# Kernel tuning notes

Measured on AMD Instinct MI355X. Metric: run time of the kernel, lower is better.

The kernel has to match this reference:

```python
import jax, jax.numpy as jnp
import numpy as np

N_NODES = 100000
N_EDGES = 1600000
D_IN = 128
CH = [128, 128]
N_GRAPHS = 256


def _glorot(key, shape):
    lim = float(np.sqrt(6.0 / (shape[0] + shape[1])))
    return jax.random.uniform(key, shape, jnp.float32, -lim, lim)


def setup_inputs() -> dict:
    key = jax.random.key(0)
    ks = jax.random.split(key, 12)
    x = jax.random.normal(ks[0], (N_NODES, D_IN), jnp.float32)
    edge_index = jax.random.randint(ks[1], (2, N_EDGES), 0, N_NODES, jnp.int64)
    batch = jnp.sort(jax.random.randint(ks[2], (N_NODES,), 0, N_GRAPHS, jnp.int64))
    W1 = _glorot(ks[3], (D_IN, CH[0]))
    b1 = jnp.zeros((CH[0],), jnp.float32)
    W2 = _glorot(ks[4], (CH[0], CH[1]))
    b2 = jnp.zeros((CH[1],), jnp.float32)
    Wm1 = _glorot(ks[5], (CH[1], 500)); bm1 = jnp.zeros((500,), jnp.float32)
    Wm2 = _glorot(ks[6], (500, 100));   bm2 = jnp.zeros((100,), jnp.float32)
    Wm3 = _glorot(ks[7], (100, 1));     bm3 = jnp.zeros((1,), jnp.float32)
    return {"x": x, "edge_index": edge_index, "batch": batch,
            "W1": W1, "b1": b1, "W2": W2, "b2": b2,
            "Wm1": Wm1, "bm1": bm1, "Wm2": Wm2, "bm2": bm2,
            "Wm3": Wm3, "bm3": bm3}


def gcn_conv(x, W, b, src, dst, n_nodes):
    # GCNConv with add_self_loops=True, symmetric normalization.
    h = x @ W  # [N, C]
    deg = jnp.zeros((n_nodes,), h.dtype).at[dst].add(1.0) + 1.0  # +1 self loop
    dinv = jax.lax.rsqrt(deg)  # deg >= 1
    norm = dinv[src] * dinv[dst]  # [E]
    agg = jnp.zeros_like(h).at[dst].add(h[src] * norm[:, None])
    agg = agg + h * (dinv * dinv)[:, None]  # self-loop term, norm = dinv[i]^2
    return agg + b


def global_mean_pool(x, batch, n_graphs):
    s = jax.ops.segment_sum(x, batch, num_segments=n_graphs)
    cnt = jax.ops.segment_sum(jnp.ones((x.shape[0],), x.dtype), batch, num_segments=n_graphs)
    return s / jnp.maximum(cnt, 1.0)[:, None]


def reference(x, edge_index, batch, W1, b1, W2, b2, Wm1, bm1, Wm2, bm2, Wm3, bm3):
    src, dst = edge_index[0], edge_index[1]
    h = jax.nn.relu(gcn_conv(x, W1, b1, src, dst, N_NODES))
    h = jax.nn.relu(gcn_conv(h, W2, b2, src, dst, N_NODES))
    g = global_mean_pool(h, batch, N_GRAPHS)  # [G, CH1]
    g = jax.nn.relu(g @ Wm1 + bm1)
    g = jax.nn.relu(g @ Wm2 + bm2)
    return g @ Wm3 + bm3  # [G, 1]
```

## Files before the change

### kernel.cpp

```cpp
#include <hip/hip_runtime.h>

#define CDIM 128
#define NGRAPH 256
#define BSH 7
#define BCAP 4096
#define NBLK 256

typedef unsigned short bf16_t;
typedef __attribute__((ext_vector_type(8))) short bf16x8;
typedef __attribute__((ext_vector_type(4))) float f32x4;

__device__ __forceinline__ float bflo(unsigned u) { return __uint_as_float(u << 16); }
__device__ __forceinline__ float bfhi(unsigned u) { return __uint_as_float(u & 0xffff0000u); }
__device__ __forceinline__ unsigned short f2bf(float f) {
  unsigned u = __float_as_uint(f);
  u += 0x7fffu + ((u >> 16) & 1u);
  return (unsigned short)(u >> 16);
}

__global__ __launch_bounds__(1024) void k_phist(const int* __restrict__ dst,
    int* __restrict__ phist, const float* __restrict__ W1,
    const float* __restrict__ W2, bf16_t* __restrict__ Wtg1,
    bf16_t* __restrict__ Wtg2, float* __restrict__ gb, int E, int NB) {
  __shared__ int hist[1024];
  int t = blockIdx.x, tid = threadIdx.x;
  int gidx = t * 1024 + tid;
  if (gidx < 16384) {
    int n = gidx >> 7, k = gidx & 127;
    Wtg1[n * 128 + k] = f2bf(W1[k * 128 + n]);
    Wtg2[n * 128 + k] = f2bf(W2[k * 128 + n]);
  }
  if (gidx < NGRAPH * CDIM) gb[gidx] = 0.f;
  for (int i = tid; i < NB; i += 1024) hist[i] = 0;
  __syncthreads();
  int tile = (E + NBLK - 1) / NBLK;
  int lo = t * tile;
  int hi = lo + tile; if (hi > E) hi = E;
  for (int i = lo + tid; i < hi; i += 1024) atomicAdd(&hist[dst[i] >> BSH], 1);
  __syncthreads();
  for (int i = tid; i < NB; i += 1024) phist[i * NBLK + t] = hist[i];
}

__global__ __launch_bounds__(256) void k_bscan(int* __restrict__ phist,
    int* __restrict__ btot) {
  __shared__ int wsum[4];
  int b = blockIdx.x;
  int tid = threadIdx.x, lane = tid & 63, wave = tid >> 6;
  int orig = phist[b * NBLK + tid];
  int v = orig;
#pragma unroll
  for (int ofs = 1; ofs < 64; ofs <<= 1) {
    int u = __shfl_up(v, ofs, 64);
    if (lane >= ofs) v += u;
  }
  if (lane == 63) wsum[wave] = v;
  __syncthreads();
  int add = 0;
#pragma unroll
  for (int w = 0; w < 3; w++) if (w < wave) add += wsum[w];
  int incl = v + add;
  phist[b * NBLK + tid] = incl - orig;
  if (tid == 255) btot[b] = incl;
}

__global__ __launch_bounds__(1024) void k_boff(const int* __restrict__ bsums,
    int* __restrict__ boffs, int G) {
  __shared__ int sh[1024];
  int tid = threadIdx.x;
  int v = (tid < G) ? bsums[tid] : 0;
  sh[tid] = v;
  __syncthreads();
  for (int ofs = 1; ofs < 1024; ofs <<= 1) {
    int u = (tid >= ofs) ? sh[tid - ofs] : 0;
    __syncthreads();
    sh[tid] += u;
    __syncthreads();
  }
  if (tid < G) boffs[tid] = sh[tid] - v;
  if (tid == G) boffs[G] = (G > 0) ? sh[G - 1] : 0;
}

__global__ __launch_bounds__(1024) void k_pscatter(const int* __restrict__ src,
    const int* __restrict__ dst, const int* __restrict__ phist,
    const int* __restrict__ bbase, unsigned* __restrict__ tmp, int E, int NB) {
  __shared__ int cur[1024];
  int t = blockIdx.x, tid = threadIdx.x;
  for (int i = tid; i < NB; i += 1024) cur[i] = bbase[i] + phist[i * NBLK + t];
  __syncthreads();
  int tile = (E + NBLK - 1) / NBLK;
  int lo = t * tile;
  int hi = lo + tile; if (hi > E) hi = E;
  for (int i = lo + tid; i < hi; i += 1024) {
    int d = dst[i];
    int p = atomicAdd(&cur[d >> BSH], 1);
    tmp[p] = (unsigned)src[i] | ((unsigned)(d & 127) << 20);
  }
}

__global__ __launch_bounds__(256) void k_csort2(const unsigned* __restrict__ tmp,
    const int* __restrict__ bbase, int* __restrict__ rowptr, float* __restrict__ dinv,
    int* __restrict__ col, int N, int NB, int E) {
  __shared__ int hist[128];
  __shared__ int sc[128];
  __shared__ int lcur[128];
  __shared__ unsigned buf[BCAP];
  int b = blockIdx.x;
  int n0 = b << BSH;
  int base = bbase[b];
  int cnt = bbase[b + 1] - base;
  int tid = threadIdx.x;
  if (tid < 128) hist[tid] = 0;
  __syncthreads();
  for (int i = tid; i < cnt; i += 256) atomicAdd(&hist[(tmp[base + i] >> 20) & 127], 1);
  __syncthreads();
  if (tid < 128) sc[tid] = hist[tid];
  __syncthreads();
  for (int ofs = 1; ofs < 128; ofs <<= 1) {
    int v = (tid < 128 && tid >= ofs) ? sc[tid - ofs] : 0;
    __syncthreads();
    if (tid < 128) sc[tid] += v;
    __syncthreads();
  }
  if (tid < 128) {
    int excl = sc[tid] - hist[tid];
    lcur[tid] = excl;
    int node = n0 + tid;
    if (node < N) {
      rowptr[node] = base + excl;
      dinv[node] = rsqrtf((float)hist[tid] + 1.0f);
    }
  }
  if (b == 0 && tid == 0) rowptr[N] = E;
  __syncthreads();
  if (cnt <= BCAP) {
    for (int i = tid; i < cnt; i += 256) {
      unsigned pk = tmp[base + i];
      int p = atomicAdd(&lcur[(pk >> 20) & 127], 1);
      buf[p] = pk & 0xFFFFFu;
    }
    __syncthreads();
    for (int i = tid; i < cnt; i += 256) col[base + i] = (int)buf[i];
  } else {
    for (int i = tid; i < cnt; i += 256) {
      unsigned pk = tmp[base + i];
      int p = atomicAdd(&lcur[(pk >> 20) & 127], 1);
      col[base + p] = (int)(pk & 0xFFFFFu);
    }
  }
}

#define WSTRIDE 136
template <int BF16IN>
__global__ __launch_bounds__(256) void k_gemm(const void* __restrict__ Ap,
    const bf16_t* __restrict__ Wtg, bf16_t* __restrict__ Co, int M) {
  __shared__ bf16_t Wt[128 * WSTRIDE];
  int tid = threadIdx.x;
  for (int c2 = tid; c2 < 2048; c2 += 256) {
    int n = c2 >> 4;
    int k8 = (c2 & 15) << 3;
    *(uint4*)&Wt[n * WSTRIDE + k8] = *(const uint4*)&Wtg[n * 128 + k8];
  }
  __syncthreads();

  int wave = tid >> 6;
  int lane = tid & 63;
  int m = lane & 15;
  int q = lane >> 4;
  int nstrips = (M + 63) >> 6;

  for (int s = blockIdx.x; s < nstrips; s += gridDim.x) {
    int rowA = s * 64 + wave * 16 + m;
    if (rowA > M - 1) rowA = M - 1;
    bf16x8 a[4];
#pragma unroll
    for (int c = 0; c < 4; c++) {
      if (BF16IN) {
        a[c] = *(const bf16x8*)((const bf16_t*)Ap + (size_t)rowA * CDIM + c * 32 + q * 8);
      } else {
        const float* ap = (const float*)Ap + (size_t)rowA * CDIM + c * 32 + q * 8;
        float4 f0 = *(const float4*)ap;
        float4 f1 = *(const float4*)(ap + 4);
        union { bf16x8 v; unsigned short u[8]; } ua;
        ua.u[0] = f2bf(f0.x); ua.u[1] = f2bf(f0.y); ua.u[2] = f2bf(f0.z); ua.u[3] = f2bf(f0.w);
        ua.u[4] = f2bf(f1.x); ua.u[5] = f2bf(f1.y); ua.u[6] = f2bf(f1.z); ua.u[7] = f2bf(f1.w);
        a[c] = ua.v;
      }
    }
#pragma unroll
    for (int t = 0; t < 8; t++) {
      f32x4 acc = {0.f, 0.f, 0.f, 0.f};
#pragma unroll
      for (int c = 0; c < 4; c++) {
        bf16x8 bv = *(const bf16x8*)&Wt[(t * 16 + m) * WSTRIDE + c * 32 + q * 8];
        acc = __builtin_amdgcn_mfma_f32_16x16x32_bf16(a[c], bv, acc, 0, 0, 0);
      }
#pragma unroll
      for (int r = 0; r < 4; r++) {
        int row = s * 64 + wave * 16 + q * 4 + r;
        if (row < M) Co[(size_t)row * CDIM + t * 16 + m] = f2bf(acc[r]);
      }
    }
  }
}

__global__ __launch_bounds__(256) void k_agg0(const bf16_t* __restrict__ t,
    const int* __restrict__ rowptr, const int* __restrict__ col,
    const float* __restrict__ dinv, const float* __restrict__ bias,
    bf16_t* __restrict__ out, int N) {
  int wave = threadIdx.x >> 6;
  int lane = threadIdx.x & 63;
  int node = blockIdx.x * 4 + wave;
  if (node >= N) return;
  const unsigned* tp = (const unsigned*)t;
  float di = dinv[node];
  unsigned sv = tp[(size_t)node * 64 + lane];
  float a0 = bflo(sv) * di;
  float a1 = bfhi(sv) * di;
  int beg = rowptr[node], end = rowptr[node + 1];
  for (int base = beg; base < end; base += 64) {
    int cnt = end - base; if (cnt > 64) cnt = 64;
    int sL = 0, wLi = 0;
    if (lane < cnt) { int s = col[base + lane]; sL = s; wLi = __float_as_int(dinv[s]); }
    int cnt8 = (cnt + 7) & ~7;
    for (int j = 0; j < cnt8; j += 8) {
      int ss[8]; float ww[8]; unsigned vv[8];
#pragma unroll
      for (int u = 0; u < 8; u++) {
        ss[u] = __builtin_amdgcn_readlane(sL, j + u);
        ww[u] = __int_as_float(__builtin_amdgcn_readlane(wLi, j + u));
      }
#pragma unroll
      for (int u = 0; u < 8; u++) vv[u] = tp[(size_t)ss[u] * 64 + lane];
#pragma unroll
      for (int u = 0; u < 8; u++) {
        a0 = fmaf(bflo(vv[u]), ww[u], a0);
        a1 = fmaf(bfhi(vv[u]), ww[u], a1);
      }
    }
  }
  float2 bb = ((const float2*)bias)[lane];
  float o0 = fmaxf(fmaf(di, a0, bb.x), 0.f);
  float o1 = fmaxf(fmaf(di, a1, bb.y), 0.f);
  ((unsigned*)out)[(size_t)node * 64 + lane] =
      ((unsigned)f2bf(o1) << 16) | f2bf(o0);
}

__global__ __launch_bounds__(256) void k_aggp(const bf16_t* __restrict__ t,
    const int* __restrict__ rowptr, const int* __restrict__ col,
    const float* __restrict__ dinv, const float* __restrict__ bias,
    const int* __restrict__ batch, float* __restrict__ gsum, int N) {
  int wave = threadIdx.x >> 6;
  int lane = threadIdx.x & 63;
  int n0 = (blockIdx.x * 4 + wave) * 16;
  if (n0 >= N) return;
  int nEnd = n0 + 16; if (nEnd > N) nEnd = N;
  const unsigned* tp = (const unsigned*)t;
  float2 bb = ((const float2*)bias)[lane];
  float p0 = 0.f, p1 = 0.f;
  int curb = batch[n0];

  for (int node = n0; node < nEnd; node++) {
    float di = dinv[node];
    unsigned sv = tp[(size_t)node * 64 + lane];
    float a0 = bflo(sv) * di;
    float a1 = bfhi(sv) * di;
    int beg = rowptr[node], end = rowptr[node + 1];
    for (int base = beg; base < end; base += 64) {
      int cnt = end - base; if (cnt > 64) cnt = 64;
      int sL = 0, wLi = 0;
      if (lane < cnt) { int s = col[base + lane]; sL = s; wLi = __float_as_int(dinv[s]); }
      int cnt8 = (cnt + 7) & ~7;
      for (int j = 0; j < cnt8; j += 8) {
        int ss[8]; float ww[8]; unsigned vv[8];
#pragma unroll
        for (int u = 0; u < 8; u++) {
          ss[u] = __builtin_amdgcn_readlane(sL, j + u);
          ww[u] = __int_as_float(__builtin_amdgcn_readlane(wLi, j + u));
        }
#pragma unroll
        for (int u = 0; u < 8; u++) vv[u] = tp[(size_t)ss[u] * 64 + lane];
#pragma unroll
        for (int u = 0; u < 8; u++) {
          a0 = fmaf(bflo(vv[u]), ww[u], a0);
          a1 = fmaf(bfhi(vv[u]), ww[u], a1);
        }
      }
    }
    float o0 = fmaxf(fmaf(di, a0, bb.x), 0.f);
    float o1 = fmaxf(fmaf(di, a1, bb.y), 0.f);
    int b = batch[node];
    if (b != curb) {
      atomicAdd(&gsum[curb * CDIM + 2 * lane], p0);
      atomicAdd(&gsum[curb * CDIM + 2 * lane + 1], p1);
      curb = b; p0 = p1 = 0.f;
    }
    p0 += __uint_as_float((unsigned)f2bf(o0) << 16);
    p1 += __uint_as_float((unsigned)f2bf(o1) << 16);
  }
  atomicAdd(&gsum[curb * CDIM + 2 * lane], p0);
  atomicAdd(&gsum[curb * CDIM + 2 * lane + 1], p1);
}

__global__ __launch_bounds__(512) void k_mlp(const float* __restrict__ g,
    const int* __restrict__ batch, int N,
    const float* __restrict__ Wm1, const float* __restrict__ bm1,
    const float* __restrict__ Wm2, const float* __restrict__ bm2,
    const float* __restrict__ wm3, const float* __restrict__ bm3,
    float* __restrict__ out) {
  __shared__ float gs[CDIM];
  __shared__ float m1s[500];
  __shared__ float m2s[100];
  int bi = blockIdx.x, tid = threadIdx.x;
  if (tid < CDIM) {
    int lo = 0, hi = N;
    while (lo < hi) { int mid = (lo + hi) >> 1; if (batch[mid] < bi) lo = mid + 1; else hi = mid; }
    int s = lo;
    lo = 0; hi = N;
    int key = bi + 1;
    while (lo < hi) { int mid = (lo + hi) >> 1; if (batch[mid] < key) lo = mid + 1; else hi = mid; }
    float inv = 1.f / fmaxf((float)(lo - s), 1.f);
    gs[tid] = g[bi * CDIM + tid] * inv;
  }
  __syncthreads();
  if (tid < 500) {
    float acc = bm1[tid];
#pragma unroll 4
    for (int k = 0; k < CDIM; k++) acc = fmaf(gs[k], Wm1[k * 500 + tid], acc);
    m1s[tid] = fmaxf(acc, 0.f);
  }
  __syncthreads();
  if (tid < 100) {
    float acc = bm2[tid];
    for (int k = 0; k < 500; k++) acc = fmaf(m1s[k], Wm2[k * 100 + tid], acc);
    m2s[tid] = fmaxf(acc, 0.f) * wm3[tid];
  }
  __syncthreads();
  if (tid < 64) {
    float v = m2s[tid] + ((tid + 64 < 100) ? m2s[tid + 64] : 0.f);
#pragma unroll
    for (int ofs = 32; ofs > 0; ofs >>= 1) v += __shfl_down(v, ofs, 64);
    if (tid == 0) out[bi] = v + bm3[0];
  }
}

static inline size_t align_up(size_t v) { return (v + 255) & ~(size_t)255; }

extern "C" void kernel_launch(void* const* d_in, const int* in_sizes, int n_in,
                              void* d_out, int out_size, void* d_ws, size_t ws_size,
                              hipStream_t stream) {
  const float* x   = (const float*)d_in[0];
  const int*   ei  = (const int*)d_in[1];
  const int*   bat = (const int*)d_in[2];
  const float* W1  = (const float*)d_in[3];
  const float* b1  = (const float*)d_in[4];
  const float* W2  = (const float*)d_in[5];
  const float* b2  = (const float*)d_in[6];
  const float* Wm1 = (const float*)d_in[7];
  const float* bm1 = (const float*)d_in[8];
  const float* Wm2 = (const float*)d_in[9];
  const float* bm2 = (const float*)d_in[10];
  const float* Wm3 = (const float*)d_in[11];
  const float* bm3 = (const float*)d_in[12];
  float* out = (float*)d_out;

  const int E = in_sizes[1] / 2;
  const int N = in_sizes[2];
  const int* src = ei;
  const int* dst = ei + E;
  const int NB = (N + 127) >> BSH;
  const int M  = NB * NBLK;

  char* p = (char*)d_ws;
  bf16_t* t    = (bf16_t*)p;   p += align_up((size_t)N * CDIM * 2);
  bf16_t* h    = (bf16_t*)p;   p += align_up((size_t)N * CDIM * 2);
  int* rowptr  = (int*)p;      p += align_up((size_t)(N + 1) * 4);
  int* colx    = (int*)p;      p += align_up((size_t)E * 4);
  unsigned* tmp= (unsigned*)p; p += align_up((size_t)E * 4);
  float* dinv  = (float*)p;    p += align_up((size_t)N * 4);
  int* phist   = (int*)p;      p += align_up((size_t)M * 4);
  int* btot    = (int*)p;      p += align_up((size_t)NB * 4);
  int* bbase   = (int*)p;      p += align_up((size_t)(NB + 1) * 4);
  bf16_t* Wtg1 = (bf16_t*)p;   p += align_up((size_t)CDIM * CDIM * 2);
  bf16_t* Wtg2 = (bf16_t*)p;   p += align_up((size_t)CDIM * CDIM * 2);
  float* gb    = (float*)p;    p += align_up((size_t)NGRAPH * CDIM * 4);
  (void)ws_size; (void)n_in; (void)out_size;

  k_phist<<<NBLK, 1024, 0, stream>>>(dst, phist, W1, W2, Wtg1, Wtg2, gb, E, NB);
  k_bscan<<<NB, 256, 0, stream>>>(phist, btot);
  k_boff<<<1, 1024, 0, stream>>>(btot, bbase, NB);
  k_pscatter<<<NBLK, 1024, 0, stream>>>(src, dst, phist, bbase, tmp, E, NB);
  k_csort2<<<NB, 256, 0, stream>>>(tmp, bbase, rowptr, dinv, colx, N, NB, E);

  k_gemm<0><<<512, 256, 0, stream>>>(x, Wtg1, t, N);
  k_agg0<<<(N + 3) / 4, 256, 0, stream>>>(t, rowptr, colx, dinv, b1, h, N);
  k_gemm<1><<<512, 256, 0, stream>>>(h, Wtg2, t, N);
  int pwaves = (N + 15) / 16;
  k_aggp<<<(pwaves + 3) / 4, 256, 0, stream>>>(t, rowptr, colx, dinv, b2,
                                               bat, gb, N);
  k_mlp<<<NGRAPH, 512, 0, stream>>>(gb, bat, N, Wm1, bm1, Wm2, bm2, Wm3, bm3, out);
}
```

Baseline: 336.0 us.

## Software-pipeline gather loads in aggregation kernels and prefetch next node's edges

Both aggregation kernels now double-buffer their 8-neighbor gather batches, so loads for the next batch are issued before the FMAs on the current batch, keeping more memory requests in flight. k_aggp also prefetches the next node's rowptr, dinv, self-feature and column/weight lanes while the current node is processed. It halves the nodes handled per wave (16 to 8), which doubles the wave count. The extra live registers for two buffers may lower occupancy, and the smaller per-wave node count means more atomic flushes to the pooled sums.

```diff
diff --git a/kernel.cpp b/kernel.cpp
--- a/kernel.cpp
+++ b/kernel.cpp
@@ -202,6 +202,26 @@
     }
   }
 }
+
+#define GISS(S, W, V, JJ) \
+  { _Pragma("unroll") for (int u = 0; u < 8; u++) { \
+      S[u] = __builtin_amdgcn_readlane(sL, (JJ) + u); \
+      W[u] = __int_as_float(__builtin_amdgcn_readlane(wLi, (JJ) + u)); } \
+    _Pragma("unroll") for (int u = 0; u < 8; u++) \
+      V[u] = tp[(size_t)S[u] * 64 + lane]; }
+#define GCON(W, V) \
+  { _Pragma("unroll") for (int u = 0; u < 8; u++) { \
+      a0 = fmaf(bflo(V[u]), W[u], a0); a1 = fmaf(bfhi(V[u]), W[u], a1); } }
+#define GBLOCK(CNT) \
+  { int nb = ((CNT) + 7) >> 3; \
+    GISS(sA, wA, vA, 0); \
+    int b_ = 1; \
+    for (; b_ + 1 < nb; b_ += 2) { \
+      GISS(sB, wB, vB, b_ * 8);       GCON(wA, vA); \
+      GISS(sA, wA, vA, (b_ + 1) * 8); GCON(wB, vB); \
+    } \
+    if (b_ < nb) { GISS(sB, wB, vB, b_ * 8); GCON(wA, vA); GCON(wB, vB); } \
+    else { GCON(wA, vA); } }
 
 __global__ __launch_bounds__(256) void k_agg0(const bf16_t* __restrict__ t,
     const int* __restrict__ rowptr, const int* __restrict__ col,
@@ -217,26 +237,13 @@
   float a0 = bflo(sv) * di;
   float a1 = bfhi(sv) * di;
   int beg = rowptr[node], end = rowptr[node + 1];
+  int sA[8]; float wA[8]; unsigned vA[8];
+  int sB[8]; float wB[8]; unsigned vB[8];
   for (int base = beg; base < end; base += 64) {
     int cnt = end - base; if (cnt > 64) cnt = 64;
     int sL = 0, wLi = 0;
     if (lane < cnt) { int s = col[base + lane]; sL = s; wLi = __float_as_int(dinv[s]); }
-    int cnt8 = (cnt + 7) & ~7;
-    for (int j = 0; j < cnt8; j += 8) {
-      int ss[8]; float ww[8]; unsigned vv[8];
-#pragma unroll
-      for (int u = 0; u < 8; u++) {
-        ss[u] = __builtin_amdgcn_readlane(sL, j + u);
-        ww[u] = __int_as_float(__builtin_amdgcn_readlane(wLi, j + u));
-      }
-#pragma unroll
-      for (int u = 0; u < 8; u++) vv[u] = tp[(size_t)ss[u] * 64 + lane];
-#pragma unroll
-      for (int u = 0; u < 8; u++) {
-        a0 = fmaf(bflo(vv[u]), ww[u], a0);
-        a1 = fmaf(bfhi(vv[u]), ww[u], a1);
-      }
-    }
+    GBLOCK(cnt);
   }
   float2 bb = ((const float2*)bias)[lane];
   float o0 = fmaxf(fmaf(di, a0, bb.x), 0.f);
@@ -251,40 +258,45 @@
     const int* __restrict__ batch, float* __restrict__ gsum, int N) {
   int wave = threadIdx.x >> 6;
   int lane = threadIdx.x & 63;
-  int n0 = (blockIdx.x * 4 + wave) * 16;
+  int n0 = (blockIdx.x * 4 + wave) * 8;
   if (n0 >= N) return;
-  int nEnd = n0 + 16; if (nEnd > N) nEnd = N;
+  int nEnd = n0 + 8; if (nEnd > N) nEnd = N;
   const unsigned* tp = (const unsigned*)t;
   float2 bb = ((const float2*)bias)[lane];
   float p0 = 0.f, p1 = 0.f;
   int curb = batch[n0];
+  int sA[8]; float wA[8]; unsigned vA[8];
+  int sB[8]; float wB[8]; unsigned vB[8];
+
+  int beg = rowptr[n0], end = rowptr[n0 + 1];
+  float di = dinv[n0];
+  unsigned sv = tp[(size_t)n0 * 64 + lane];
+  int sL = 0, wLi = 0;
+  { int c0 = end - beg; if (c0 > 64) c0 = 64;
+    if (lane < c0) { int s = col[beg + lane]; sL = s; wLi = __float_as_int(dinv[s]); } }
 
   for (int node = n0; node < nEnd; node++) {
-    float di = dinv[node];
-    unsigned sv = tp[(size_t)node * 64 + lane];
     float a0 = bflo(sv) * di;
     float a1 = bfhi(sv) * di;
-    int beg = rowptr[node], end = rowptr[node + 1];
-    for (int base = beg; base < end; base += 64) {
+    int nn = node + 1;
+    int begN = 0, endN = 0, sLN = 0, wLiN = 0;
+    float diN = 0.f; unsigned svN = 0;
+    if (nn < nEnd) {
+      begN = rowptr[nn]; endN = rowptr[nn + 1];
+      diN = dinv[nn];
+      svN = tp[(size_t)nn * 64 + lane];
+      int c0 = endN - begN; if (c0 > 64) c0 = 64;
+      if (lane < c0) { int s = col[begN + lane]; sLN = s; wLiN = __float_as_int(dinv[s]); }
+    }
+    {
+      int cnt = end - beg; if (cnt > 64) cnt = 64;
+      GBLOCK(cnt);
+    }
+    for (int base = beg + 64; base < end; base += 64) {
       int cnt = end - base; if (cnt > 64) cnt = 64;
-      int sL = 0, wLi = 0;
+      sL = 0; wLi = 0;
       if (lane < cnt) { int s = col[base + lane]; sL = s; wLi = __float_as_int(dinv[s]); }
-      int cnt8 = (cnt + 7) & ~7;
-      for (int j = 0; j < cnt8; j += 8) {
-        int ss[8]; float ww[8]; unsigned vv[8];
-#pragma unroll
-        for (int u = 0; u < 8; u++) {
-          ss[u] = __builtin_amdgcn_readlane(sL, j + u);
-          ww[u] = __int_as_float(__builtin_amdgcn_readlane(wLi, j + u));
-        }
-#pragma unroll
-        for (int u = 0; u < 8; u++) vv[u] = tp[(size_t)ss[u] * 64 + lane];
-#pragma unroll
-        for (int u = 0; u < 8; u++) {
-          a0 = fmaf(bflo(vv[u]), ww[u], a0);
-          a1 = fmaf(bfhi(vv[u]), ww[u], a1);
-        }
-      }
+      GBLOCK(cnt);
     }
     float o0 = fmaxf(fmaf(di, a0, bb.x), 0.f);
     float o1 = fmaxf(fmaf(di, a1, bb.y), 0.f);
@@ -296,6 +308,7 @@
     }
     p0 += __uint_as_float((unsigned)f2bf(o0) << 16);
     p1 += __uint_as_float((unsigned)f2bf(o1) << 16);
+    beg = begN; end = endN; di = diN; sv = svN; sL = sLN; wLi = wLiN;
   }
   atomicAdd(&gsum[curb * CDIM + 2 * lane], p0);
   atomicAdd(&gsum[curb * CDIM + 2 * lane + 1], p1);
@@ -394,7 +407,7 @@
   k_gemm<0><<<512, 256, 0, stream>>>(x, Wtg1, t, N);
   k_agg0<<<(N + 3) / 4, 256, 0, stream>>>(t, rowptr, colx, dinv, b1, h, N);
   k_gemm<1><<<512, 256, 0, stream>>>(h, Wtg2, t, N);
-  int pwaves = (N + 15) / 16;
+  int pwaves = (N + 7) / 8;
   k_aggp<<<(pwaves + 3) / 4, 256, 0, stream>>>(t, rowptr, colx, dinv, b2,
                                                bat, gb, N);
   k_mlp<<<NGRAPH, 512, 0, stream>>>(gb, bat, N, Wm1, bm1, Wm2, bm2, Wm3, bm3, out);
```

Result: no change. 341.6 us (+1.7%).

## Split aggregation into feature slices with half-wave edge pairing and persistent grid

Applied to the files above, without the earlier changes.

Both aggregation kernels now run each wave on a 64-column feature slice, chosen by block parity, so each 128-byte row read is half as wide. Each half-wave handles alternate edges and the two halves are combined with a cross-lane shuffle. Gathers are software-pipelined with double-buffered register sets, and the launch becomes a fixed 2048-block grid-stride loop. The aim is more memory-level parallelism and better cache locality per feature slice. The cost is that every node's neighbor indices and dinv values are read twice, once per slice, plus extra shuffle and readlane work.

```diff
diff --git a/kernel.cpp b/kernel.cpp
--- a/kernel.cpp
+++ b/kernel.cpp
@@ -203,46 +203,69 @@
   }
 }
 
+#define GISS(W, V, JJ) \
+  { _Pragma("unroll") for (int r = 0; r < 4; r++) { \
+      int e0 = (JJ) + 2 * r; \
+      int sa = __builtin_amdgcn_readlane(sL, e0); \
+      int sb = __builtin_amdgcn_readlane(sL, e0 + 1); \
+      int wa = __builtin_amdgcn_readlane(wLi, e0); \
+      int wb = __builtin_amdgcn_readlane(wLi, e0 + 1); \
+      int se = g ? sb : sa; \
+      W[r] = __int_as_float(g ? wb : wa); \
+      V[r] = tp2[(size_t)se * 64 + widx]; \
+  } }
+#define GCON(W, V) \
+  { _Pragma("unroll") for (int r = 0; r < 4; r++) { \
+      a0 = fmaf(bflo(V[r]), W[r], a0); a1 = fmaf(bfhi(V[r]), W[r], a1); } }
+#define GBLOCK(CNT) \
+  { int nb_ = ((CNT) + 7) >> 3; \
+    GISS(wA, vA, 0); \
+    int b_ = 1; \
+    for (; b_ + 1 < nb_; b_ += 2) { \
+      GISS(wB, vB, b_ * 8);       GCON(wA, vA); \
+      GISS(wA, vA, (b_ + 1) * 8); GCON(wB, vB); \
+    } \
+    if (b_ < nb_) { GISS(wB, vB, b_ * 8); GCON(wA, vA); GCON(wB, vB); } \
+    else { GCON(wA, vA); } }
+
 __global__ __launch_bounds__(256) void k_agg0(const bf16_t* __restrict__ t,
     const int* __restrict__ rowptr, const int* __restrict__ col,
     const float* __restrict__ dinv, const float* __restrict__ bias,
     bf16_t* __restrict__ out, int N) {
   int wave = threadIdx.x >> 6;
   int lane = threadIdx.x & 63;
-  int node = blockIdx.x * 4 + wave;
-  if (node >= N) return;
-  const unsigned* tp = (const unsigned*)t;
-  float di = dinv[node];
-  unsigned sv = tp[(size_t)node * 64 + lane];
-  float a0 = bflo(sv) * di;
-  float a1 = bfhi(sv) * di;
-  int beg = rowptr[node], end = rowptr[node + 1];
-  for (int base = beg; base < end; base += 64) {
-    int cnt = end - base; if (cnt > 64) cnt = 64;
-    int sL = 0, wLi = 0;
-    if (lane < cnt) { int s = col[base + lane]; sL = s; wLi = __float_as_int(dinv[s]); }
-    int cnt8 = (cnt + 7) & ~7;
-    for (int j = 0; j < cnt8; j += 8) {
-      int ss[8]; float ww[8]; unsigned vv[8];
-#pragma unroll
-      for (int u = 0; u < 8; u++) {
-        ss[u] = __builtin_amdgcn_readlane(sL, j + u);
-        ww[u] = __int_as_float(__builtin_amdgcn_readlane(wLi, j + u));
-      }
-#pragma unroll
-      for (int u = 0; u < 8; u++) vv[u] = tp[(size_t)ss[u] * 64 + lane];
-#pragma unroll
-      for (int u = 0; u < 8; u++) {
-        a0 = fmaf(bflo(vv[u]), ww[u], a0);
-        a1 = fmaf(bfhi(vv[u]), ww[u], a1);
-      }
-    }
-  }
-  float2 bb = ((const float2*)bias)[lane];
-  float o0 = fmaxf(fmaf(di, a0, bb.x), 0.f);
-  float o1 = fmaxf(fmaf(di, a1, bb.y), 0.f);
-  ((unsigned*)out)[(size_t)node * 64 + lane] =
-      ((unsigned)f2bf(o1) << 16) | f2bf(o0);
+  int slice = blockIdx.x & 1;
+  int g = lane >> 5;
+  int widx = lane & 31;
+  const unsigned* tp2 = (const unsigned*)t + slice * 32;
+  float wA[4]; unsigned vA[4];
+  float wB[4]; unsigned vB[4];
+  int step = gridDim.x >> 1;
+  for (int nb = blockIdx.x >> 1; nb * 4 < N; nb += step) {
+    int node = nb * 4 + wave;
+    if (node >= N) continue;
+    float di = dinv[node];
+    unsigned sv = tp2[(size_t)node * 64 + widx];
+    float sw = (g == 0) ? di : 0.f;
+    float a0 = bflo(sv) * sw;
+    float a1 = bfhi(sv) * sw;
+    int beg = rowptr[node], end = rowptr[node + 1];
+    for (int base = beg; base < end; base += 64) {
+      int cnt = end - base; if (cnt > 64) cnt = 64;
+      int sL = 0, wLi = 0;
+      if (lane < cnt) { int s = col[base + lane]; sL = s; wLi = __float_as_int(dinv[s]); }
+      GBLOCK(cnt);
+    }
+    a0 += __shfl_xor(a0, 32, 64);
+    a1 += __shfl_xor(a1, 32, 64);
+    if (g == 0) {
+      float2 bb = ((const float2*)bias)[slice * 32 + widx];
+      float o0 = fmaxf(fmaf(di, a0, bb.x), 0.f);
+      float o1 = fmaxf(fmaf(di, a1, bb.y), 0.f);
+      ((unsigned*)out)[(size_t)node * 64 + slice * 32 + widx] =
+          ((unsigned)f2bf(o1) << 16) | f2bf(o0);
+    }
+  }
 }
 
 __global__ __launch_bounds__(256) void k_aggp(const bf16_t* __restrict__ t,
@@ -251,54 +274,55 @@
     const int* __restrict__ batch, float* __restrict__ gsum, int N) {
   int wave = threadIdx.x >> 6;
   int lane = threadIdx.x & 63;
-  int n0 = (blockIdx.x * 4 + wave) * 16;
-  if (n0 >= N) return;
-  int nEnd = n0 + 16; if (nEnd > N) nEnd = N;
-  const unsigned* tp = (const unsigned*)t;
-  float2 bb = ((const float2*)bias)[lane];
-  float p0 = 0.f, p1 = 0.f;
-  int curb = batch[n0];
-
-  for (int node = n0; node < nEnd; node++) {
-    float di = dinv[node];
-    unsigned sv = tp[(size_t)node * 64 + lane];
-    float a0 = bflo(sv) * di;
-    float a1 = bfhi(sv) * di;
-    int beg = rowptr[node], end = rowptr[node + 1];
-    for (int base = beg; base < end; base += 64) {
-      int cnt = end - base; if (cnt > 64) cnt = 64;
-      int sL = 0, wLi = 0;
-      if (lane < cnt) { int s = col[base + lane]; sL = s; wLi = __float_as_int(dinv[s]); }
-      int cnt8 = (cnt + 7) & ~7;
-      for (int j = 0; j < cnt8; j += 8) {
-        int ss[8]; float ww[8]; unsigned vv[8];
-#pragma unroll
-        for (int u = 0; u < 8; u++) {
-          ss[u] = __builtin_amdgcn_readlane(sL, j + u);
-          ww[u] = __int_as_float(__builtin_amdgcn_readlane(wLi, j + u));
+  int slice = blockIdx.x & 1;
+  int g = lane >> 5;
+  int widx = lane & 31;
+  const unsigned* tp2 = (const unsigned*)t + slice * 32;
+  float2 bb = ((const float2*)bias)[slice * 32 + widx];
+  float wA[4]; unsigned vA[4];
+  float wB[4]; unsigned vB[4];
+  int T = (N + 15) >> 4;
+  int step = gridDim.x >> 1;
+  for (int nb = blockIdx.x >> 1; nb * 4 < T; nb += step) {
+    int task = nb * 4 + wave;
+    if (task >= T) continue;
+    int n0 = task * 16;
+    int nEnd = n0 + 16; if (nEnd > N) nEnd = N;
+    float p0 = 0.f, p1 = 0.f;
+    int curb = batch[n0];
+    for (int node = n0; node < nEnd; node++) {
+      float di = dinv[node];
+      unsigned sv = tp2[(size_t)node * 64 + widx];
+      float sw = (g == 0) ? di : 0.f;
+      float a0 = bflo(sv) * sw;
+      float a1 = bfhi(sv) * sw;
+      int beg = rowptr[node], end = rowptr[node + 1];
+      for (int base = beg; base < end; base += 64) {
+        int cnt = end - base; if (cnt > 64) cnt = 64;
+        int sL = 0, wLi = 0;
+        if (lane < cnt) { int s = col[base + lane]; sL = s; wLi = __float_as_int(dinv[s]); }
+        GBLOCK(cnt);
+      }
+      a0 += __shfl_xor(a0, 32, 64);
+      a1 += __shfl_xor(a1, 32, 64);
+      float o0 = fmaxf(fmaf(di, a0, bb.x), 0.f);
+      float o1 = fmaxf(fmaf(di, a1, bb.y), 0.f);
+      int b = batch[node];
+      if (b != curb) {
+        if (g == 0) {
+          atomicAdd(&gsum[curb * CDIM + slice * 64 + 2 * widx], p0);
+          atomicAdd(&gsum[curb * CDIM + slice * 64 + 2 * widx + 1], p1);
         }
-#pragma unroll
-        for (int u = 0; u < 8; u++) vv[u] = tp[(size_t)ss[u] * 64 + lane];
-#pragma unroll
-        for (int u = 0; u < 8; u++) {
-          a0 = fmaf(bflo(vv[u]), ww[u], a0);
-          a1 = fmaf(bfhi(vv[u]), ww[u], a1);
-        }
+        curb = b; p0 = p1 = 0.f;
       }
-    }
-    float o0 = fmaxf(fmaf(di, a0, bb.x), 0.f);
-    float o1 = fmaxf(fmaf(di, a1, bb.y), 0.f);
-    int b = batch[node];
-    if (b != curb) {
-      atomicAdd(&gsum[curb * CDIM + 2 * lane], p0);
-      atomicAdd(&gsum[curb * CDIM + 2 * lane + 1], p1);
-      curb = b; p0 = p1 = 0.f;
-    }
-    p0 += __uint_as_float((unsigned)f2bf(o0) << 16);
-    p1 += __uint_as_float((unsigned)f2bf(o1) << 16);
-  }
-  atomicAdd(&gsum[curb * CDIM + 2 * lane], p0);
-  atomicAdd(&gsum[curb * CDIM + 2 * lane + 1], p1);
+      p0 += __uint_as_float((unsigned)f2bf(o0) << 16);
+      p1 += __uint_as_float((unsigned)f2bf(o1) << 16);
+    }
+    if (g == 0) {
+      atomicAdd(&gsum[curb * CDIM + slice * 64 + 2 * widx], p0);
+      atomicAdd(&gsum[curb * CDIM + slice * 64 + 2 * widx + 1], p1);
+    }
+  }
 }
 
 __global__ __launch_bounds__(512) void k_mlp(const float* __restrict__ g,
@@ -392,10 +416,8 @@
   k_csort2<<<NB, 256, 0, stream>>>(tmp, bbase, rowptr, dinv, colx, N, NB, E);
 
   k_gemm<0><<<512, 256, 0, stream>>>(x, Wtg1, t, N);
-  k_agg0<<<(N + 3) / 4, 256, 0, stream>>>(t, rowptr, colx, dinv, b1, h, N);
+  k_agg0<<<2048, 256, 0, stream>>>(t, rowptr, colx, dinv, b1, h, N);
   k_gemm<1><<<512, 256, 0, stream>>>(h, Wtg2, t, N);
-  int pwaves = (N + 15) / 16;
-  k_aggp<<<(pwaves + 3) / 4, 256, 0, stream>>>(t, rowptr, colx, dinv, b2,
-                                               bat, gb, N);
+  k_aggp<<<2048, 256, 0, stream>>>(t, rowptr, colx, dinv, b2, bat, gb, N);
   k_mlp<<<NGRAPH, 512, 0, stream>>>(gb, bat, N, Wm1, bm1, Wm2, bm2, Wm3, bm3, out);
 }
```

Result: slower. 420.2 us (+25.1%).

## Prescale GEMM output by dinv and software-pipeline neighbor gathers with zero sentinel row

Applied to the files above, without the earlier changes.

The GEMM epilogue now multiplies each output row by dinv[row], so the aggregation kernels sum pre-normalized neighbor rows without loading dinv[src] or doing per-edge FMAs. Padding lanes point to a zeroed sentinel row N, which removes per-edge weight reads and masking. The gather loop is double-buffered so the loads of the next 8 neighbors are issued before the current 8 are accumulated, to hide memory latency. Rounding changes slightly because scaling happens before the bf16 store, and one extra row of workspace is used.

```diff
diff --git a/kernel.cpp b/kernel.cpp
--- a/kernel.cpp
+++ b/kernel.cpp
@@ -21,7 +21,8 @@
 __global__ __launch_bounds__(1024) void k_phist(const int* __restrict__ dst,
     int* __restrict__ phist, const float* __restrict__ W1,
     const float* __restrict__ W2, bf16_t* __restrict__ Wtg1,
-    bf16_t* __restrict__ Wtg2, float* __restrict__ gb, int E, int NB) {
+    bf16_t* __restrict__ Wtg2, float* __restrict__ gb, bf16_t* __restrict__ tz,
+    int N, int E, int NB) {
   __shared__ int hist[1024];
   int t = blockIdx.x, tid = threadIdx.x;
   int gidx = t * 1024 + tid;
@@ -31,6 +32,7 @@
     Wtg2[n * 128 + k] = f2bf(W2[k * 128 + n]);
   }
   if (gidx < NGRAPH * CDIM) gb[gidx] = 0.f;
+  if (gidx < 64) ((unsigned*)(tz + (size_t)N * CDIM))[gidx] = 0u;
   for (int i = tid; i < NB; i += 1024) hist[i] = 0;
   __syncthreads();
   int tile = (E + NBLK - 1) / NBLK;
@@ -152,7 +154,8 @@
 #define WSTRIDE 136
 template <int BF16IN>
 __global__ __launch_bounds__(256) void k_gemm(const void* __restrict__ Ap,
-    const bf16_t* __restrict__ Wtg, bf16_t* __restrict__ Co, int M) {
+    const bf16_t* __restrict__ Wtg, const float* __restrict__ dscale,
+    bf16_t* __restrict__ Co, int M) {
   __shared__ bf16_t Wt[128 * WSTRIDE];
   int tid = threadIdx.x;
   for (int c2 = tid; c2 < 2048; c2 += 256) {
@@ -186,6 +189,12 @@
         a[c] = ua.v;
       }
     }
+    float sc[4];
+#pragma unroll
+    for (int r = 0; r < 4; r++) {
+      int row = s * 64 + wave * 16 + q * 4 + r;
+      sc[r] = (row < M) ? dscale[row] : 0.f;
+    }
 #pragma unroll
     for (int t = 0; t < 8; t++) {
       f32x4 acc = {0.f, 0.f, 0.f, 0.f};
@@ -197,11 +206,30 @@
 #pragma unroll
       for (int r = 0; r < 4; r++) {
         int row = s * 64 + wave * 16 + q * 4 + r;
-        if (row < M) Co[(size_t)row * CDIM + t * 16 + m] = f2bf(acc[r]);
+        if (row < M) Co[(size_t)row * CDIM + t * 16 + m] = f2bf(acc[r] * sc[r]);
       }
     }
   }
 }
+
+#define GISS(S, V, JJ) \
+  { _Pragma("unroll") for (int u = 0; u < 8; u++) \
+      S[u] = __builtin_amdgcn_readlane(sL, (JJ) + u); \
+    _Pragma("unroll") for (int u = 0; u < 8; u++) \
+      V[u] = tp[(size_t)S[u] * 64 + lane]; }
+#define GCON(V) \
+  { _Pragma("unroll") for (int u = 0; u < 8; u++) { \
+      a0 += bflo(V[u]); a1 += bfhi(V[u]); } }
+#define GBLOCK(CNT) \
+  { int nb = ((CNT) + 7) >> 3; \
+    GISS(sA, vA, 0); \
+    int b_ = 1; \
+    for (; b_ + 1 < nb; b_ += 2) { \
+      GISS(sB, vB, b_ * 8);       GCON(vA); \
+      GISS(sA, vA, (b_ + 1) * 8); GCON(vB); \
+    } \
+    if (b_ < nb) { GISS(sB, vB, b_ * 8); GCON(vA); GCON(vB); } \
+    else { GCON(vA); } }
 
 __global__ __launch_bounds__(256) void k_agg0(const bf16_t* __restrict__ t,
     const int* __restrict__ rowptr, const int* __restrict__ col,
@@ -214,29 +242,16 @@
   const unsigned* tp = (const unsigned*)t;
   float di = dinv[node];
   unsigned sv = tp[(size_t)node * 64 + lane];
-  float a0 = bflo(sv) * di;
-  float a1 = bfhi(sv) * di;
+  float a0 = bflo(sv);
+  float a1 = bfhi(sv);
   int beg = rowptr[node], end = rowptr[node + 1];
+  int sA[8]; unsigned vA[8];
+  int sB[8]; unsigned vB[8];
   for (int base = beg; base < end; base += 64) {
     int cnt = end - base; if (cnt > 64) cnt = 64;
-    int sL = 0, wLi = 0;
-    if (lane < cnt) { int s = col[base + lane]; sL = s; wLi = __float_as_int(dinv[s]); }
-    int cnt8 = (cnt + 7) & ~7;
-    for (int j = 0; j < cnt8; j += 8) {
-      int ss[8]; float ww[8]; unsigned vv[8];
-#pragma unroll
-      for (int u = 0; u < 8; u++) {
-        ss[u] = __builtin_amdgcn_readlane(sL, j + u);
-        ww[u] = __int_as_float(__builtin_amdgcn_readlane(wLi, j + u));
-      }
-#pragma unroll
-      for (int u = 0; u < 8; u++) vv[u] = tp[(size_t)ss[u] * 64 + lane];
-#pragma unroll
-      for (int u = 0; u < 8; u++) {
-        a0 = fmaf(bflo(vv[u]), ww[u], a0);
-        a1 = fmaf(bfhi(vv[u]), ww[u], a1);
-      }
-    }
+    int sL = N;
+    if (lane < cnt) sL = col[base + lane];
+    GBLOCK(cnt);
   }
   float2 bb = ((const float2*)bias)[lane];
   float o0 = fmaxf(fmaf(di, a0, bb.x), 0.f);
@@ -258,33 +273,20 @@
   float2 bb = ((const float2*)bias)[lane];
   float p0 = 0.f, p1 = 0.f;
   int curb = batch[n0];
+  int sA[8]; unsigned vA[8];
+  int sB[8]; unsigned vB[8];
 
   for (int node = n0; node < nEnd; node++) {
     float di = dinv[node];
     unsigned sv = tp[(size_t)node * 64 + lane];
-    float a0 = bflo(sv) * di;
-    float a1 = bfhi(sv) * di;
+    float a0 = bflo(sv);
+    float a1 = bfhi(sv);
     int beg = rowptr[node], end = rowptr[node + 1];
     for (int base = beg; base < end; base += 64) {
       int cnt = end - base; if (cnt > 64) cnt = 64;
-      int sL = 0, wLi = 0;
-      if (lane < cnt) { int s = col[base + lane]; sL = s; wLi = __float_as_int(dinv[s]); }
-      int cnt8 = (cnt + 7) & ~7;
-      for (int j = 0; j < cnt8; j += 8) {
-        int ss[8]; float ww[8]; unsigned vv[8];
-#pragma unroll
-        for (int u = 0; u < 8; u++) {
-          ss[u] = __builtin_amdgcn_readlane(sL, j + u);
-          ww[u] = __int_as_float(__builtin_amdgcn_readlane(wLi, j + u));
-        }
-#pragma unroll
-        for (int u = 0; u < 8; u++) vv[u] = tp[(size_t)ss[u] * 64 + lane];
-#pragma unroll
-        for (int u = 0; u < 8; u++) {
-          a0 = fmaf(bflo(vv[u]), ww[u], a0);
-          a1 = fmaf(bfhi(vv[u]), ww[u], a1);
-        }
-      }
+      int sL = N;
+      if (lane < cnt) sL = col[base + lane];
+      GBLOCK(cnt);
     }
     float o0 = fmaxf(fmaf(di, a0, bb.x), 0.f);
     float o1 = fmaxf(fmaf(di, a1, bb.y), 0.f);
@@ -371,7 +373,7 @@
   const int M  = NB * NBLK;
 
   char* p = (char*)d_ws;
-  bf16_t* t    = (bf16_t*)p;   p += align_up((size_t)N * CDIM * 2);
+  bf16_t* t    = (bf16_t*)p;   p += align_up((size_t)(N + 1) * CDIM * 2);
   bf16_t* h    = (bf16_t*)p;   p += align_up((size_t)N * CDIM * 2);
   int* rowptr  = (int*)p;      p += align_up((size_t)(N + 1) * 4);
   int* colx    = (int*)p;      p += align_up((size_t)E * 4);
@@ -385,15 +387,15 @@
   float* gb    = (float*)p;    p += align_up((size_t)NGRAPH * CDIM * 4);
   (void)ws_size; (void)n_in; (void)out_size;
 
-  k_phist<<<NBLK, 1024, 0, stream>>>(dst, phist, W1, W2, Wtg1, Wtg2, gb, E, NB);
+  k_phist<<<NBLK, 1024, 0, stream>>>(dst, phist, W1, W2, Wtg1, Wtg2, gb, t, N, E, NB);
   k_bscan<<<NB, 256, 0, stream>>>(phist, btot);
   k_boff<<<1, 1024, 0, stream>>>(btot, bbase, NB);
   k_pscatter<<<NBLK, 1024, 0, stream>>>(src, dst, phist, bbase, tmp, E, NB);
   k_csort2<<<NB, 256, 0, stream>>>(tmp, bbase, rowptr, dinv, colx, N, NB, E);
 
-  k_gemm<0><<<512, 256, 0, stream>>>(x, Wtg1, t, N);
+  k_gemm<0><<<512, 256, 0, stream>>>(x, Wtg1, dinv, t, N);
   k_agg0<<<(N + 3) / 4, 256, 0, stream>>>(t, rowptr, colx, dinv, b1, h, N);
-  k_gemm<1><<<512, 256, 0, stream>>>(h, Wtg2, t, N);
+  k_gemm<1><<<512, 256, 0, stream>>>(h, Wtg2, dinv, t, N);
   int pwaves = (N + 15) / 16;
   k_aggp<<<(pwaves + 3) / 4, 256, 0, stream>>>(t, rowptr, colx, dinv, b2,
                                                bat, gb, N);
```

Result: faster. 328.2 us (-2.3%).
